# Optimization experiments

Hardware: AMD Instinct MI355X
Metric: run time of the kernel (lower is better)

Reference implementation:

```python
import jax, jax.numpy as jnp
import numpy as np

BLOCK = 32  # GGML Q8_0-style block size: one scale per 32 quantized values


def setup_inputs() -> dict:
    key = jax.random.key(0)
    k1, k2, k3, k4 = jax.random.split(key, 4)
    B, S, IN, OUT = 2, 4096, 4096, 4096
    inp = jax.random.normal(k1, (B, S, IN), dtype=jnp.float32)
    # stored GGUF layout: [in_features, out_features]; torch forward transposes it
    qweight = jax.random.randint(k2, (IN, OUT), -127, 128, dtype=jnp.int32)  # int8 codes
    scales = jax.random.normal(k3, (IN, OUT // BLOCK), dtype=jnp.float32) * 0.01  # per-block scale
    bias = jax.random.normal(k4, (OUT,), dtype=jnp.float32) * 0.02
    return {"input": inp, "qweight": qweight, "scales": scales, "bias": bias}


def _dequantize(qweight, scales, dtype):
    # blockwise dequant: w[i, b*32 + j] = q[i, b*32 + j] * scale[i, b]
    IN, OUT = qweight.shape
    q = qweight.reshape(IN, OUT // BLOCK, BLOCK).astype(dtype)
    return (q * scales[:, :, None].astype(dtype)).reshape(IN, OUT)


def reference(input, qweight, scales, bias):
    # torch: F.linear(x, W_stored.T, b) == x @ W_stored + b with W_stored [IN, OUT]
    w = _dequantize(qweight, scales, input.dtype)  # [IN, OUT]
    return jnp.einsum('bsi,io->bso', input, w) + bias
```

## Files before the change

kernel.cpp:

```cpp
#include <hip/hip_runtime.h>
#include <stdint.h>


#define M_DIM 8192
#define N_DIM 4096
#define K_DIM 4096
#define NBLK  128
#define NT    128

typedef __attribute__((ext_vector_type(8))) short short8;
typedef __attribute__((ext_vector_type(4))) float f32x4;

typedef const __attribute__((address_space(1))) unsigned char* gas;
typedef __attribute__((address_space(3))) unsigned char* las;

__device__ __forceinline__ unsigned pk_bf16(float a, float b) {
  unsigned ua = __builtin_bit_cast(unsigned, a);
  unsigned ub = __builtin_bit_cast(unsigned, b);
  ua += 0x7fffu + ((ua >> 16) & 1u);
  ub += 0x7fffu + ((ub >> 16) & 1u);
  return (ua >> 16) | (ub & 0xffff0000u);
}

__global__ __launch_bounds__(256)
void a_to_bf16(const float* __restrict__ A, ushort* __restrict__ Abf) {
  const long idx = ((long)blockIdx.x * 256 + threadIdx.x) * 8;
  const float4 v0 = *(const float4*)(A + idx);
  const float4 v1 = *(const float4*)(A + idx + 4);
  uint4 p;
  p.x = pk_bf16(v0.x, v0.y);
  p.y = pk_bf16(v0.z, v0.w);
  p.z = pk_bf16(v1.x, v1.y);
  p.w = pk_bf16(v1.z, v1.w);
  *(uint4*)(Abf + idx) = p;
}

__global__ __launch_bounds__(256)
void dequant_transpose(const int* __restrict__ Q, const float* __restrict__ S,
                       ushort* __restrict__ Wt) {
  __shared__ ushort T[64 * 68];
  const int k0 = blockIdx.y * 64;
  const int n0 = blockIdx.x * 64;
  const int t = threadIdx.x;
  const int nl = t & 63;
  const int kb = t >> 6;

  #pragma unroll
  for (int i = 0; i < 16; ++i) {
    const int kl = kb + i * 4;
    const int k = k0 + kl;
    const int q = Q[(long)k * N_DIM + n0 + nl];
    const float s = S[k * NBLK + ((n0 + nl) >> 5)];
    const float w = (float)q * s;
    unsigned u = __builtin_bit_cast(unsigned, w);
    u += 0x7fffu + ((u >> 16) & 1u);
    T[nl * 68 + kl] = (ushort)(u >> 16);
  }
  __syncthreads();

  const int n = t >> 2;
  const int kc = (t & 3) * 16;
  const ushort* src = &T[n * 68 + kc];
  uint2 a = *(const uint2*)(src + 0);
  uint2 b = *(const uint2*)(src + 4);
  uint2 c = *(const uint2*)(src + 8);
  uint2 d = *(const uint2*)(src + 12);
  uint4 o0 = {a.x, a.y, b.x, b.y};
  uint4 o1 = {c.x, c.y, d.x, d.y};
  ushort* dst = Wt + (long)(n0 + n) * K_DIM + k0 + kc;
  *(uint4*)(dst + 0) = o0;
  *(uint4*)(dst + 8) = o1;
}

__global__ __launch_bounds__(512, 2)
void gemm256(const ushort* __restrict__ Abf, const ushort* __restrict__ Wt,
             const float* __restrict__ bias, float* __restrict__ C) {
  __shared__ __align__(16) ushort lds[4 * 16384];

  const int tid = threadIdx.x;
  const int wave = tid >> 6, lane = tid & 63;
  const int lrow = lane & 15, quad = lane >> 4;

  int id = (int)blockIdx.x;
  id = (id & 7) * 64 + (id >> 3);
  const int m0 = (id >> 4) * 256;
  const int n0 = (id & 15) * 256;

  const int wm = (wave >> 2) * 128;
  const int wn = (wave & 3) * 64;
  const int rchunk = (quad ^ ((lrow >> 1) & 3)) * 8;

  const int srow = lane >> 2;
  const int schunk = ((lane & 3) ^ ((lane >> 3) & 3)) * 8;
  const ushort* Ag0 = Abf + (long)(m0 + wave * 16 + srow) * K_DIM + schunk;
  const ushort* Ag1 = Ag0 + (long)128 * K_DIM;
  const ushort* Bg0 = Wt  + (long)(n0 + wave * 16 + srow) * K_DIM + schunk;
  const ushort* Bg1 = Bg0 + (long)128 * K_DIM;

  f32x4 acc[8][4];
  #pragma unroll
  for (int i = 0; i < 8; ++i)
    #pragma unroll
    for (int j = 0; j < 4; ++j)
      acc[i][j] = (f32x4){0.f, 0.f, 0.f, 0.f};

#define STAGE(kt, ss) do {                                                   \
    const long ko_ = (long)(kt) * 32;                                        \
    ushort* As_ = (ushort*)&lds[(ss) * 16384];                               \
    __builtin_amdgcn_global_load_lds((gas)(Ag0 + ko_),                       \
        (las)(As_ + wave * 512), 16, 0, 0);                                  \
    __builtin_amdgcn_global_load_lds((gas)(Ag1 + ko_),                       \
        (las)(As_ + 4096 + wave * 512), 16, 0, 0);                           \
    __builtin_amdgcn_global_load_lds((gas)(Bg0 + ko_),                       \
        (las)(As_ + 8192 + wave * 512), 16, 0, 0);                           \
    __builtin_amdgcn_global_load_lds((gas)(Bg1 + ko_),                       \
        (las)(As_ + 12288 + wave * 512), 16, 0, 0);                          \
  } while (0)

#define COMPUTE(s_) do {                                                     \
    const ushort* As_ = (const ushort*)&lds[(s_) * 16384];                   \
    const ushort* Bs_ = As_ + 8192;                                          \
    short8 af[8], bf[4];                                                     \
    _Pragma("unroll")                                                        \
    for (int mt = 0; mt < 8; ++mt)                                           \
      af[mt] = *(const short8*)&As_[(wm + mt * 16 + lrow) * 32 + rchunk];    \
    _Pragma("unroll")                                                        \
    for (int nt2 = 0; nt2 < 4; ++nt2)                                        \
      bf[nt2] = *(const short8*)&Bs_[(wn + nt2 * 16 + lrow) * 32 + rchunk];  \
    __builtin_amdgcn_s_setprio(1);                                           \
    _Pragma("unroll")                                                        \
    for (int mt = 0; mt < 8; ++mt)                                           \
      _Pragma("unroll")                                                      \
      for (int nt2 = 0; nt2 < 4; ++nt2)                                      \
        acc[mt][nt2] = __builtin_amdgcn_mfma_f32_16x16x32_bf16(              \
            af[mt], bf[nt2], acc[mt][nt2], 0, 0, 0);                         \
    __builtin_amdgcn_s_setprio(0);                                           \
  } while (0)

#define SYNC(n_) do {                                                        \
    asm volatile("s_waitcnt vmcnt(" #n_ ")" ::: "memory");                   \
    __builtin_amdgcn_s_barrier();                                            \
    __builtin_amdgcn_sched_barrier(0);                                       \
  } while (0)

  STAGE(0, 0);
  STAGE(1, 1);
  STAGE(2, 2);
  SYNC(8);

  #pragma unroll 1
  for (int t = 0; t < NT - 4; t += 4) {
    STAGE(t + 3, 3); COMPUTE(0); SYNC(8);
    STAGE(t + 4, 0); COMPUTE(1); SYNC(8);
    STAGE(t + 5, 1); COMPUTE(2); SYNC(8);
    STAGE(t + 6, 2); COMPUTE(3); SYNC(8);
  }
  STAGE(127, 3); COMPUTE(0); SYNC(8);
  COMPUTE(1); SYNC(4);
  COMPUTE(2); SYNC(0);
  COMPUTE(3);

#undef STAGE
#undef COMPUTE
#undef SYNC

  #pragma unroll
  for (int nt2 = 0; nt2 < 4; ++nt2) {
    const int n = n0 + wn + nt2 * 16 + lrow;
    const float bv = bias[n];
    #pragma unroll
    for (int mt = 0; mt < 8; ++mt) {
      const int mbase = m0 + wm + mt * 16 + quad * 4;
      #pragma unroll
      for (int r = 0; r < 4; ++r)
        C[(long)(mbase + r) * N_DIM + n] = acc[mt][nt2][r] + bv;
    }
  }
}

__global__ __launch_bounds__(256)
void gguf_gemm_fused(const float* __restrict__ A, const int* __restrict__ Q,
                     const float* __restrict__ S, const float* __restrict__ bias,
                     float* __restrict__ C) {
  __shared__ __align__(16) ushort Alds[128 * 32];
  __shared__ __align__(16) ushort Blds[128 * 32];
  const int tid = threadIdx.x;
  const int m0 = blockIdx.y * 128;
  const int n0 = blockIdx.x * 128;
  const int wave = tid >> 6, lane = tid & 63;
  const int wm = (wave >> 1) * 64, wn = (wave & 1) * 64;
  const int lrow = lane & 15, quad = lane >> 4;
  const int ar = tid >> 2, ac = (tid & 3) * 4;
  const int c8a = ((ar >> 1) & 3) << 3;
  const int bn = tid & 127, bkc = (tid >> 7) * 16;
  const int c8b = ((bn >> 1) & 3) << 3;
  const float* Abase = A + (long)(m0 + ar) * K_DIM + ac;
  const int* Qbase = Q + (long)bkc * N_DIM + n0 + bn;
  const float* Sbase = S + (long)bkc * NBLK + ((n0 + bn) >> 5);
  f32x4 acc[4][4];
  #pragma unroll
  for (int i = 0; i < 4; ++i)
    #pragma unroll
    for (int j = 0; j < 4; ++j) acc[i][j] = (f32x4){0.f, 0.f, 0.f, 0.f};
  for (int k0 = 0; k0 < K_DIM; k0 += 32) {
    #pragma unroll
    for (int i = 0; i < 2; ++i)
      #pragma unroll
      for (int j = 0; j < 2; ++j) {
        const float4 v = *(const float4*)(Abase + (long)i * 64 * K_DIM + k0 + j * 16);
        uint2 p; p.x = pk_bf16(v.x, v.y); p.y = pk_bf16(v.z, v.w);
        const int k = ac + j * 16;
        *(uint2*)&Alds[(ar + i * 64) * 32 + (k ^ c8a)] = p;
      }
    {
      const int* qp = Qbase + (long)k0 * N_DIM;
      const float* sp = Sbase + (long)k0 * NBLK;
      unsigned w[8];
      #pragma unroll
      for (int i = 0; i < 8; ++i) {
        const int q0 = qp[(2 * i) * N_DIM];
        const int q1 = qp[(2 * i + 1) * N_DIM];
        const float s0 = sp[(2 * i) * NBLK];
        const float s1 = sp[(2 * i + 1) * NBLK];
        w[i] = pk_bf16((float)q0 * s0, (float)q1 * s1);
      }
      uint4 g0 = {w[0], w[1], w[2], w[3]};
      uint4 g1 = {w[4], w[5], w[6], w[7]};
      *(uint4*)&Blds[bn * 32 + (bkc ^ c8b)] = g0;
      *(uint4*)&Blds[bn * 32 + ((bkc + 8) ^ c8b)] = g1;
    }
    __syncthreads();
    short8 afrag[4], bfrag[4];
    #pragma unroll
    for (int t = 0; t < 4; ++t) {
      const int mrow = wm + t * 16 + lrow;
      afrag[t] = *(const short8*)&Alds[mrow * 32 + ((quad * 8) ^ (((mrow >> 1) & 3) << 3))];
      const int nrow = wn + t * 16 + lrow;
      bfrag[t] = *(const short8*)&Blds[nrow * 32 + ((quad * 8) ^ (((nrow >> 1) & 3) << 3))];
    }
    #pragma unroll
    for (int mt = 0; mt < 4; ++mt)
      #pragma unroll
      for (int nt = 0; nt < 4; ++nt)
        acc[mt][nt] = __builtin_amdgcn_mfma_f32_16x16x32_bf16(afrag[mt], bfrag[nt],
                                                              acc[mt][nt], 0, 0, 0);
    __syncthreads();
  }
  #pragma unroll
  for (int nt = 0; nt < 4; ++nt) {
    const int n = n0 + wn + nt * 16 + lrow;
    const float bv = bias[n];
    #pragma unroll
    for (int mt = 0; mt < 4; ++mt) {
      const int mbase = m0 + wm + mt * 16 + quad * 4;
      #pragma unroll
      for (int r = 0; r < 4; ++r)
        C[(long)(mbase + r) * N_DIM + n] = acc[mt][nt][r] + bv;
    }
  }
}

extern "C" void kernel_launch(void* const* d_in, const int* in_sizes, int n_in,
                              void* d_out, int out_size, void* d_ws, size_t ws_size,
                              hipStream_t stream) {
  const float* A    = (const float*)d_in[0];
  const int*   Q    = (const int*)d_in[1];
  const float* S    = (const float*)d_in[2];
  const float* bias = (const float*)d_in[3];
  float* C = (float*)d_out;

  const size_t abf_bytes = (size_t)M_DIM * K_DIM * 2;
  const size_t wt_bytes  = (size_t)N_DIM * K_DIM * 2;

  if (ws_size >= abf_bytes + wt_bytes) {
    ushort* Abf = (ushort*)d_ws;
    ushort* Wt  = (ushort*)((char*)d_ws + abf_bytes);
    a_to_bf16<<<(M_DIM * (long)K_DIM) / (256 * 8), 256, 0, stream>>>(A, Abf);
    dim3 gt(N_DIM / 64, K_DIM / 64);
    dequant_transpose<<<gt, 256, 0, stream>>>(Q, S, Wt);
    gemm256<<<dim3((M_DIM / 256) * (N_DIM / 256)), dim3(512), 0, stream>>>(Abf, Wt, bias, C);
  } else {
    dim3 grid(N_DIM / 128, M_DIM / 128);
    gguf_gemm_fused<<<grid, 256, 0, stream>>>(A, Q, S, bias, C);
  }
}
```

Baseline: 513.3 us.

## Split K-tile compute into two half-phases interleaving loads and remap block-to-XCD tiles

Each K-step now runs in two phases of 16 MFMAs. The A and B global-to-LDS stage loads are issued separately between those phases, with extra barriers so LDS reads, loads and MFMAs interleave more finely. This is meant to overlap memory issue with compute and to cut register pressure, since only 4 A fragments are live at a time. The block index mapping also changes so each XCD covers a 4x2 group of 8x8-tile regions, to improve L2 reuse of A and B per XCD. The cost is more s_barrier calls per K-step.

```diff
diff --git a/kernel.cpp b/kernel.cpp
--- a/kernel.cpp
+++ b/kernel.cpp
@@ -81,10 +81,11 @@
   const int wave = tid >> 6, lane = tid & 63;
   const int lrow = lane & 15, quad = lane >> 4;
 
-  int id = (int)blockIdx.x;
-  id = (id & 7) * 64 + (id >> 3);
-  const int m0 = (id >> 4) * 256;
-  const int n0 = (id & 15) * 256;
+  const int id = (int)blockIdx.x;
+  const int xcd = id & 7;
+  const int j = id >> 3;
+  const int m0 = ((xcd & 3) * 8 + (j & 7)) * 256;
+  const int n0 = ((xcd >> 2) * 8 + (j >> 3)) * 256;
 
   const int wm = (wave >> 2) * 128;
   const int wn = (wave & 3) * 64;
@@ -101,68 +102,101 @@
   #pragma unroll
   for (int i = 0; i < 8; ++i)
     #pragma unroll
-    for (int j = 0; j < 4; ++j)
-      acc[i][j] = (f32x4){0.f, 0.f, 0.f, 0.f};
-
-#define STAGE(kt, ss) do {                                                   \
-    const long ko_ = (long)(kt) * 32;                                        \
-    ushort* As_ = (ushort*)&lds[(ss) * 16384];                               \
-    __builtin_amdgcn_global_load_lds((gas)(Ag0 + ko_),                       \
-        (las)(As_ + wave * 512), 16, 0, 0);                                  \
-    __builtin_amdgcn_global_load_lds((gas)(Ag1 + ko_),                       \
-        (las)(As_ + 4096 + wave * 512), 16, 0, 0);                           \
-    __builtin_amdgcn_global_load_lds((gas)(Bg0 + ko_),                       \
-        (las)(As_ + 8192 + wave * 512), 16, 0, 0);                           \
-    __builtin_amdgcn_global_load_lds((gas)(Bg1 + ko_),                       \
-        (las)(As_ + 12288 + wave * 512), 16, 0, 0);                          \
+    for (int j2 = 0; j2 < 4; ++j2)
+      acc[i][j2] = (f32x4){0.f, 0.f, 0.f, 0.f};
+
+#define STAGE_A(kt, ss) do {                                                 \
+    const long koa_ = (long)(kt) * 32;                                       \
+    ushort* Ad_ = (ushort*)&lds[(ss) * 16384];                               \
+    __builtin_amdgcn_global_load_lds((gas)(Ag0 + koa_),                      \
+        (las)(Ad_ + wave * 512), 16, 0, 0);                                  \
+    __builtin_amdgcn_global_load_lds((gas)(Ag1 + koa_),                      \
+        (las)(Ad_ + 4096 + wave * 512), 16, 0, 0);                           \
   } while (0)
 
-#define COMPUTE(s_) do {                                                     \
-    const ushort* As_ = (const ushort*)&lds[(s_) * 16384];                   \
-    const ushort* Bs_ = As_ + 8192;                                          \
-    short8 af[8], bf[4];                                                     \
-    _Pragma("unroll")                                                        \
-    for (int mt = 0; mt < 8; ++mt)                                           \
-      af[mt] = *(const short8*)&As_[(wm + mt * 16 + lrow) * 32 + rchunk];    \
+#define STAGE_B(kt, ss) do {                                                 \
+    const long kob_ = (long)(kt) * 32;                                       \
+    ushort* Bd_ = (ushort*)&lds[(ss) * 16384 + 8192];                        \
+    __builtin_amdgcn_global_load_lds((gas)(Bg0 + kob_),                      \
+        (las)(Bd_ + wave * 512), 16, 0, 0);                                  \
+    __builtin_amdgcn_global_load_lds((gas)(Bg1 + kob_),                      \
+        (las)(Bd_ + 4096 + wave * 512), 16, 0, 0);                           \
+  } while (0)
+
+#define VM8 asm volatile("s_waitcnt vmcnt(8)" ::: "memory")
+#define VM4 asm volatile("s_waitcnt vmcnt(4)" ::: "memory")
+#define VM0 asm volatile("s_waitcnt vmcnt(0)" ::: "memory")
+#define NOP ((void)0)
+
+#define TILE(s_, SA_, SB_, VMW_) do {                                        \
+    const ushort* Asl_ = (const ushort*)&lds[(s_) * 16384];                  \
+    const ushort* Bsl_ = Asl_ + 8192;                                        \
+    short8 af_[4], a2_[4], bf_[4];                                           \
+    _Pragma("unroll")                                                        \
+    for (int mt = 0; mt < 4; ++mt)                                           \
+      af_[mt] = *(const short8*)&Asl_[(wm + mt * 16 + lrow) * 32 + rchunk];  \
     _Pragma("unroll")                                                        \
     for (int nt2 = 0; nt2 < 4; ++nt2)                                        \
-      bf[nt2] = *(const short8*)&Bs_[(wn + nt2 * 16 + lrow) * 32 + rchunk];  \
+      bf_[nt2] = *(const short8*)&Bsl_[(wn + nt2 * 16 + lrow) * 32 + rchunk];\
+    SA_;                                                                     \
+    __builtin_amdgcn_s_barrier();                                            \
+    asm volatile("s_waitcnt lgkmcnt(0)" ::: "memory");                       \
+    __builtin_amdgcn_sched_barrier(0);                                       \
     __builtin_amdgcn_s_setprio(1);                                           \
     _Pragma("unroll")                                                        \
-    for (int mt = 0; mt < 8; ++mt)                                           \
+    for (int mt = 0; mt < 4; ++mt)                                           \
       _Pragma("unroll")                                                      \
       for (int nt2 = 0; nt2 < 4; ++nt2)                                      \
         acc[mt][nt2] = __builtin_amdgcn_mfma_f32_16x16x32_bf16(              \
-            af[mt], bf[nt2], acc[mt][nt2], 0, 0, 0);                         \
+            af_[mt], bf_[nt2], acc[mt][nt2], 0, 0, 0);                       \
     __builtin_amdgcn_s_setprio(0);                                           \
-  } while (0)
-
-#define SYNC(n_) do {                                                        \
-    asm volatile("s_waitcnt vmcnt(" #n_ ")" ::: "memory");                   \
+    __builtin_amdgcn_s_barrier();                                            \
+    _Pragma("unroll")                                                        \
+    for (int mt = 0; mt < 4; ++mt)                                           \
+      a2_[mt] = *(const short8*)&Asl_[(wm + 64 + mt * 16 + lrow) * 32 + rchunk]; \
+    SB_;                                                                     \
+    VMW_;                                                                    \
+    __builtin_amdgcn_s_barrier();                                            \
+    asm volatile("s_waitcnt lgkmcnt(0)" ::: "memory");                       \
+    __builtin_amdgcn_sched_barrier(0);                                       \
+    __builtin_amdgcn_s_setprio(1);                                           \
+    _Pragma("unroll")                                                        \
+    for (int mt = 0; mt < 4; ++mt)                                           \
+      _Pragma("unroll")                                                      \
+      for (int nt2 = 0; nt2 < 4; ++nt2)                                      \
+        acc[mt + 4][nt2] = __builtin_amdgcn_mfma_f32_16x16x32_bf16(          \
+            a2_[mt], bf_[nt2], acc[mt + 4][nt2], 0, 0, 0);                   \
+    __builtin_amdgcn_s_setprio(0);                                           \
     __builtin_amdgcn_s_barrier();                                            \
     __builtin_amdgcn_sched_barrier(0);                                       \
   } while (0)
 
-  STAGE(0, 0);
-  STAGE(1, 1);
-  STAGE(2, 2);
-  SYNC(8);
+  STAGE_A(0, 0); STAGE_B(0, 0);
+  STAGE_A(1, 1); STAGE_B(1, 1);
+  STAGE_A(2, 2); STAGE_B(2, 2);
+  VM8;
+  __builtin_amdgcn_s_barrier();
+  __builtin_amdgcn_sched_barrier(0);
 
   #pragma unroll 1
   for (int t = 0; t < NT - 4; t += 4) {
-    STAGE(t + 3, 3); COMPUTE(0); SYNC(8);
-    STAGE(t + 4, 0); COMPUTE(1); SYNC(8);
-    STAGE(t + 5, 1); COMPUTE(2); SYNC(8);
-    STAGE(t + 6, 2); COMPUTE(3); SYNC(8);
-  }
-  STAGE(127, 3); COMPUTE(0); SYNC(8);
-  COMPUTE(1); SYNC(4);
-  COMPUTE(2); SYNC(0);
-  COMPUTE(3);
-
-#undef STAGE
-#undef COMPUTE
-#undef SYNC
+    TILE(0, STAGE_A(t + 3, 3), STAGE_B(t + 3, 3), VM8);
+    TILE(1, STAGE_A(t + 4, 0), STAGE_B(t + 4, 0), VM8);
+    TILE(2, STAGE_A(t + 5, 1), STAGE_B(t + 5, 1), VM8);
+    TILE(3, STAGE_A(t + 6, 2), STAGE_B(t + 6, 2), VM8);
+  }
+  TILE(0, STAGE_A(127, 3), STAGE_B(127, 3), VM8);
+  TILE(1, NOP, NOP, VM4);
+  TILE(2, NOP, NOP, VM0);
+  TILE(3, NOP, NOP, NOP);
+
+#undef STAGE_A
+#undef STAGE_B
+#undef TILE
+#undef VM8
+#undef VM4
+#undef VM0
+#undef NOP
 
   #pragma unroll
   for (int nt2 = 0; nt2 < 4; ++nt2) {
```

Result: faster. 496.8 us (-3.2%).
